# Kernel optimization log

Hardware: AMD Instinct MI355X
Metric: run time of the kernel (lower is better)

The kernel has to match this reference:

```python
import jax, jax.numpy as jnp
import numpy as np

HIDDEN = 2048
INTER = 8192
RETRIEVAL = 128
NUM_EXPERTS = 4096
NUM_KEYS = 64  # sqrt(NUM_EXPERTS)
TOP_K = 8
B, S = 4, 2048


def setup_inputs() -> dict:
    key = jax.random.key(0)
    ks = jax.random.split(key, 8)
    sc = 0.02
    return {
        "hidden_states": jax.random.normal(ks[0], (B, S, HIDDEN), jnp.float32),
        "W_q": jax.random.normal(ks[1], (HIDDEN, RETRIEVAL), jnp.float32) * sc,
        "keys": jax.random.normal(ks[2], (2, RETRIEVAL // 2, NUM_KEYS), jnp.float32) * sc,
        "down_embed": jax.random.normal(ks[3], (NUM_EXPERTS, HIDDEN), jnp.float32) * sc,
        "up_embed": jax.random.normal(ks[4], (NUM_EXPERTS, HIDDEN), jnp.float32) * sc,
        "gate_w": jax.random.normal(ks[5], (HIDDEN, INTER), jnp.float32) * sc,
        "up_w": jax.random.normal(ks[6], (HIDDEN, INTER), jnp.float32) * sc,
        "down_w": jax.random.normal(ks[7], (INTER, HIDDEN), jnp.float32) * sc,
    }


def reference(hidden_states, W_q, keys, down_embed, up_embed, gate_w, up_w, down_w):
    b, s, h = hidden_states.shape
    n = b * s
    # product-key routing (faithful to the source's view(2, N, -1) reshape)
    queries = (hidden_states @ W_q).reshape(2, n, RETRIEVAL // 2)  # [2, N, rd/2]
    routing = jnp.einsum('tnd,tdk->tnk', queries, keys)            # [2, N, num_keys]
    scores2, idx2 = jax.lax.top_k(routing, TOP_K)                  # [2, N, k]
    sx, sy = scores2[0], scores2[1]
    ix, iy = idx2[0], idx2[1]
    all_scores = (sx[:, :, None] + sy[:, None, :]).reshape(n, TOP_K * TOP_K)
    all_idx = (ix[:, :, None] * NUM_KEYS + iy[:, None, :]).reshape(n, TOP_K * TOP_K)
    scores, pk = jax.lax.top_k(all_scores, TOP_K)                  # [N, k]
    indices = jnp.take_along_axis(all_idx, pk, axis=-1)            # [N, k]
    # expert embedding gather + per-token tiny matmuls
    de = down_embed[indices]                                       # [N, k, H]
    ue = up_embed[indices]                                         # [N, k, H]
    x = hidden_states.reshape(n, h)
    ew = jnp.einsum('nh,nkh->nk', x, de)                           # [N, k]
    ew = jax.nn.silu(ew) * jax.nn.softmax(scores, axis=-1)
    experts_states = jnp.einsum('nk,nkh->nh', ew, ue).reshape(b, s, h)
    # dense SwiGLU MLP branch
    mlp = (jax.nn.silu(x @ gate_w) * (x @ up_w)) @ down_w
    return mlp.reshape(b, s, h) + experts_states
```

## Files before the change

kernel.cpp:

```cpp
#include <hip/hip_runtime.h>
#include <cstdint>
#include <cstddef>

#define HIDDEN 2048
#define INTER 8192
#define NTOK 8192
#define RET 128
#define NKEYS 64
#define TOPK 8

typedef __bf16 bf16_t;
typedef bf16_t bf16x8 __attribute__((ext_vector_type(8)));
typedef float floatx4 __attribute__((ext_vector_type(4)));

#define BARRIER() asm volatile("s_barrier" ::: "memory")
#define WAIT_LGKM0()                                     \
  do {                                                   \
    asm volatile("s_waitcnt lgkmcnt(0)" ::: "memory");   \
    __builtin_amdgcn_sched_barrier(0);                   \
  } while (0)
#define WAIT_VM8() asm volatile("s_waitcnt vmcnt(8)" ::: "memory")
#define WAIT_VM4() asm volatile("s_waitcnt vmcnt(4)" ::: "memory")
#define WAIT_VM0() asm volatile("s_waitcnt vmcnt(0)" ::: "memory")

__device__ inline void tile_end_wait(int rem) {
  if (rem >= 3) WAIT_VM8();
  else if (rem == 2) WAIT_VM4();
  else if (rem == 1) WAIT_VM0();
}

__device__ inline unsigned short f2bf(float f) {
  union { float f; unsigned u; } v; v.f = f;
  unsigned r = v.u + 0x7FFFu + ((v.u >> 16) & 1u);
  return (unsigned short)(r >> 16);
}

__device__ inline void gld_lds16(unsigned short* lds, const unsigned short* g) {
  auto* l3 = reinterpret_cast<__attribute__((address_space(3))) unsigned int*>(
      reinterpret_cast<uintptr_t>(lds));
  auto* g1 = reinterpret_cast<const __attribute__((address_space(1))) unsigned int*>(
      reinterpret_cast<uintptr_t>(g));
  __builtin_amdgcn_global_load_lds(g1, l3, 16, 0, 0);
}

__device__ inline void xcd_map(int gx, int gy, int& bx, int& by) {
  if ((gx & 7) != 0) return;
  int lin = by * gx + bx;
  int W = gx >> 3;
  int xcd = lin & 7;
  int j = lin >> 3;
  int r = j / W, c = j % W;
  if (r & 1) c = W - 1 - c;
  bx = xcd * W + c;
  by = r;
}

__device__ inline void stage_op256(unsigned short* ldsbuf, const unsigned short* g,
                                   int rows0, int K, int kt, int tid, int wid) {
#pragma unroll
  for (int i = 0; i < 2; ++i) {
    int c = i * 512 + tid;
    int row = c >> 2;
    int cc = (c & 3) ^ (row & 3) ^ ((row >> 2) & 3);
    gld_lds16(ldsbuf + (size_t)(i * 512 + wid * 64) * 8,
              g + (size_t)(rows0 + row) * K + kt + cc * 8);
  }
}
__device__ inline void stage_op128(unsigned short* ldsbuf, const unsigned short* g,
                                   int rows0, int K, int kt, int tid, int wid) {
  int row = tid >> 2;
  int cc = (tid & 3) ^ (row & 3) ^ ((row >> 2) & 3);
  gld_lds16(ldsbuf + (size_t)(wid * 64) * 8,
            g + (size_t)(rows0 + row) * K + kt + cc * 8);
}

__global__ __launch_bounds__(256) void cvt_bf16(const float* __restrict__ in,
                                                unsigned short* __restrict__ out,
                                                int count4) {
  for (int i = blockIdx.x * blockDim.x + threadIdx.x; i < count4;
       i += gridDim.x * blockDim.x) {
    float4 v = reinterpret_cast<const float4*>(in)[i];
    ushort4 o;
    o.x = f2bf(v.x); o.y = f2bf(v.y); o.z = f2bf(v.z); o.w = f2bf(v.w);
    reinterpret_cast<ushort4*>(out)[i] = o;
  }
}

__global__ __launch_bounds__(256) void transpose_cvt(const float* __restrict__ in,
                                                     unsigned short* __restrict__ out,
                                                     int R, int C) {
  __shared__ float tile[32][33];
  int c0 = blockIdx.x * 32, r0 = blockIdx.y * 32;
  int tx = threadIdx.x, ty = threadIdx.y;
#pragma unroll
  for (int it = 0; it < 4; ++it)
    tile[ty + it * 8][tx] = in[(size_t)(r0 + ty + it * 8) * C + c0 + tx];
  __syncthreads();
#pragma unroll
  for (int it = 0; it < 4; ++it)
    out[(size_t)(c0 + ty + it * 8) * R + r0 + tx] = f2bf(tile[tx][ty + it * 8]);
}

enum { EPI_F32 = 0, EPI_ADDF32 = 3 };

template <int MODE>
__global__ __launch_bounds__(256) void gemm_bt(const unsigned short* __restrict__ A,
                                               const unsigned short* __restrict__ B,
                                               float* __restrict__ Cf,
                                               int M, int N, int K) {
  __shared__ unsigned short As[128 * 64];
  __shared__ unsigned short Bs[128 * 64];
  const int tid = threadIdx.x;
  const int lane = tid & 63, wid = tid >> 6;
  const int wm = wid >> 1, wn = wid & 1;
  int bx = blockIdx.x, by = blockIdx.y;
  xcd_map(gridDim.x, gridDim.y, bx, by);
  const int m0 = by * 128, n0 = bx * 128;
  const int lr = lane & 15, q = lane >> 4;
  const int swz = lr & 7;

  floatx4 acc[4][4];
#pragma unroll
  for (int i = 0; i < 4; ++i)
#pragma unroll
    for (int j = 0; j < 4; ++j) acc[i][j] = (floatx4){0.f, 0.f, 0.f, 0.f};

  for (int k0 = 0; k0 < K; k0 += 64) {
#pragma unroll
    for (int s = 0; s < 4; ++s) {
      int c = s * 256 + wid * 64 + lane;
      int row = c >> 3, cc = (c & 7) ^ (row & 7);
      gld_lds16(&As[(s * 256 + wid * 64) * 8],
                A + (size_t)(m0 + row) * K + k0 + cc * 8);
      gld_lds16(&Bs[(s * 256 + wid * 64) * 8],
                B + (size_t)(n0 + row) * K + k0 + cc * 8);
    }
    __syncthreads();
#pragma unroll
    for (int kc = 0; kc < 2; ++kc) {
      const int coff = ((kc * 4 + q) ^ swz) * 8;
      bf16x8 af[4], bfv[4];
#pragma unroll
      for (int t = 0; t < 4; ++t) {
        af[t] = *reinterpret_cast<const bf16x8*>(
            &As[(wm * 64 + t * 16 + lr) * 64 + coff]);
        bfv[t] = *reinterpret_cast<const bf16x8*>(
            &Bs[(wn * 64 + t * 16 + lr) * 64 + coff]);
      }
#pragma unroll
      for (int i = 0; i < 4; ++i)
#pragma unroll
        for (int j = 0; j < 4; ++j)
          acc[i][j] = __builtin_amdgcn_mfma_f32_16x16x32_bf16(af[i], bfv[j],
                                                              acc[i][j], 0, 0, 0);
    }
    __syncthreads();
  }

#pragma unroll
  for (int i = 0; i < 4; ++i) {
    int rbase = m0 + wm * 64 + i * 16 + q * 4;
#pragma unroll
    for (int j = 0; j < 4; ++j) {
      int col = n0 + wn * 64 + j * 16 + lr;
#pragma unroll
      for (int r = 0; r < 4; ++r) {
        size_t idx = (size_t)(rbase + r) * N + col;
        float v = acc[i][j][r];
        if (MODE == EPI_F32) Cf[idx] = v;
        else Cf[idx] = v + Cf[idx];
      }
    }
  }
}

template <int MODE>
__global__ __launch_bounds__(512, 2) void gemm256(const unsigned short* __restrict__ A,
                                                  const unsigned short* __restrict__ B,
                                                  float* __restrict__ Cf,
                                                  int N, int K) {
  extern __shared__ unsigned short sm[];
  const int tid = threadIdx.x;
  const int lane = tid & 63, wid = tid >> 6;
  const int wm = wid >> 2, wn = wid & 3;
  int bx = blockIdx.x, by = blockIdx.y;
  xcd_map(gridDim.x, gridDim.y, bx, by);
  const int m0 = by * 256, n0 = bx * 256;
  const int lr = lane & 15, q = lane >> 4;
  const int swz = (lr & 3) ^ ((lr >> 2) & 3);
  const int coff = (q ^ swz) * 8;
  unsigned short* Abase = sm;
  unsigned short* Bbase = sm + 32768;
  const int NT = K >> 5;

  floatx4 acc[8][4];
#pragma unroll
  for (int i = 0; i < 8; ++i)
#pragma unroll
    for (int j = 0; j < 4; ++j) acc[i][j] = (floatx4){0.f, 0.f, 0.f, 0.f};

#pragma unroll
  for (int tt = 0; tt < 3; ++tt) {
    stage_op256(Abase + tt * 8192, A, m0, K, tt * 32, tid, wid);
    stage_op256(Bbase + tt * 8192, B, n0, K, tt * 32, tid, wid);
  }
  WAIT_VM8();
  BARRIER();

  for (int t = 0; t < NT; ++t) {
    const int buf = t & 3;
    const unsigned short* As = Abase + buf * 8192;
    const unsigned short* Bs = Bbase + buf * 8192;
    bf16x8 af[4], bfv[4];
#pragma unroll
    for (int m = 0; m < 4; ++m)
      af[m] = *reinterpret_cast<const bf16x8*>(
          &As[(wm * 128 + m * 16 + lr) * 32 + coff]);
#pragma unroll
    for (int n = 0; n < 4; ++n)
      bfv[n] = *reinterpret_cast<const bf16x8*>(
          &Bs[(wn * 64 + n * 16 + lr) * 32 + coff]);
    if (t + 3 < NT)
      stage_op256(Abase + ((t + 3) & 3) * 8192, A, m0, K, (t + 3) * 32, tid, wid);
    BARRIER();
    WAIT_LGKM0();
    __builtin_amdgcn_s_setprio(1);
#pragma unroll
    for (int m = 0; m < 4; ++m)
#pragma unroll
      for (int n = 0; n < 4; ++n)
        acc[m][n] = __builtin_amdgcn_mfma_f32_16x16x32_bf16(af[m], bfv[n],
                                                            acc[m][n], 0, 0, 0);
    __builtin_amdgcn_s_setprio(0);
    __builtin_amdgcn_sched_barrier(0);
    BARRIER();
#pragma unroll
    for (int m = 0; m < 4; ++m)
      af[m] = *reinterpret_cast<const bf16x8*>(
          &As[(wm * 128 + (m + 4) * 16 + lr) * 32 + coff]);
    if (t + 3 < NT)
      stage_op256(Bbase + ((t + 3) & 3) * 8192, B, n0, K, (t + 3) * 32, tid, wid);
    BARRIER();
    WAIT_LGKM0();
    __builtin_amdgcn_s_setprio(1);
#pragma unroll
    for (int m = 0; m < 4; ++m)
#pragma unroll
      for (int n = 0; n < 4; ++n)
        acc[m + 4][n] = __builtin_amdgcn_mfma_f32_16x16x32_bf16(af[m], bfv[n],
                                                                acc[m + 4][n], 0, 0, 0);
    __builtin_amdgcn_s_setprio(0);
    __builtin_amdgcn_sched_barrier(0);
    tile_end_wait(NT - 1 - t);
    BARRIER();
  }

#pragma unroll
  for (int m = 0; m < 8; ++m) {
    int rbase = m0 + wm * 128 + m * 16 + q * 4;
#pragma unroll
    for (int n = 0; n < 4; ++n) {
      int col = n0 + wn * 64 + n * 16 + lr;
#pragma unroll
      for (int r = 0; r < 4; ++r) {
        size_t idx = (size_t)(rbase + r) * N + col;
        float v = acc[m][n][r];
        if (MODE == EPI_F32) Cf[idx] = v;
        else Cf[idx] = v + Cf[idx];
      }
    }
  }
}

__global__ __launch_bounds__(512, 2) void gateup256(const unsigned short* __restrict__ A,
                                                    const unsigned short* __restrict__ Bg,
                                                    const unsigned short* __restrict__ Bu,
                                                    unsigned short* __restrict__ H,
                                                    int N, int K) {
  extern __shared__ unsigned short sm[];
  const int tid = threadIdx.x;
  const int lane = tid & 63, wid = tid >> 6;
  const int wm = wid >> 1, wn = wid & 1;
  int bx = blockIdx.x, by = blockIdx.y;
  xcd_map(gridDim.x, gridDim.y, bx, by);
  const int m0 = by * 256, n0 = bx * 128;
  const int lr = lane & 15, q = lane >> 4;
  const int swz = (lr & 3) ^ ((lr >> 2) & 3);
  const int coff = (q ^ swz) * 8;
  unsigned short* Abase = sm;
  unsigned short* Bgbase = sm + 32768;
  unsigned short* Bubase = sm + 49152;
  const int NT = K >> 5;

  floatx4 accg[4][4], accu[4][4];
#pragma unroll
  for (int i = 0; i < 4; ++i)
#pragma unroll
    for (int j = 0; j < 4; ++j) {
      accg[i][j] = (floatx4){0.f, 0.f, 0.f, 0.f};
      accu[i][j] = (floatx4){0.f, 0.f, 0.f, 0.f};
    }

#pragma unroll
  for (int tt = 0; tt < 3; ++tt) {
    stage_op256(Abase + tt * 8192, A, m0, K, tt * 32, tid, wid);
    stage_op128(Bgbase + tt * 4096, Bg, n0, K, tt * 32, tid, wid);
    stage_op128(Bubase + tt * 4096, Bu, n0, K, tt * 32, tid, wid);
  }
  WAIT_VM8();
  BARRIER();

  for (int t = 0; t < NT; ++t) {
    const int buf = t & 3;
    const unsigned short* As = Abase + buf * 8192;
    const unsigned short* Bgs = Bgbase + buf * 4096;
    const unsigned short* Bus = Bubase + buf * 4096;
    bf16x8 af[2], bg[4], bu[4];
#pragma unroll
    for (int m = 0; m < 2; ++m)
      af[m] = *reinterpret_cast<const bf16x8*>(
          &As[(wm * 64 + m * 16 + lr) * 32 + coff]);
#pragma unroll
    for (int n = 0; n < 4; ++n) {
      bg[n] = *reinterpret_cast<const bf16x8*>(
          &Bgs[(wn * 64 + n * 16 + lr) * 32 + coff]);
      bu[n] = *reinterpret_cast<const bf16x8*>(
          &Bus[(wn * 64 + n * 16 + lr) * 32 + coff]);
    }
    if (t + 3 < NT)
      stage_op256(Abase + ((t + 3) & 3) * 8192, A, m0, K, (t + 3) * 32, tid, wid);
    BARRIER();
    WAIT_LGKM0();
    __builtin_amdgcn_s_setprio(1);
#pragma unroll
    for (int m = 0; m < 2; ++m)
#pragma unroll
      for (int n = 0; n < 4; ++n) {
        accg[m][n] = __builtin_amdgcn_mfma_f32_16x16x32_bf16(af[m], bg[n],
                                                             accg[m][n], 0, 0, 0);
        accu[m][n] = __builtin_amdgcn_mfma_f32_16x16x32_bf16(af[m], bu[n],
                                                             accu[m][n], 0, 0, 0);
      }
    __builtin_amdgcn_s_setprio(0);
    __builtin_amdgcn_sched_barrier(0);
    BARRIER();
#pragma unroll
    for (int m = 0; m < 2; ++m)
      af[m] = *reinterpret_cast<const bf16x8*>(
          &As[(wm * 64 + (m + 2) * 16 + lr) * 32 + coff]);
    if (t + 3 < NT) {
      stage_op128(Bgbase + ((t + 3) & 3) * 4096, Bg, n0, K, (t + 3) * 32, tid, wid);
      stage_op128(Bubase + ((t + 3) & 3) * 4096, Bu, n0, K, (t + 3) * 32, tid, wid);
    }
    BARRIER();
    WAIT_LGKM0();
    __builtin_amdgcn_s_setprio(1);
#pragma unroll
    for (int m = 0; m < 2; ++m)
#pragma unroll
      for (int n = 0; n < 4; ++n) {
        accg[m + 2][n] = __builtin_amdgcn_mfma_f32_16x16x32_bf16(af[m], bg[n],
                                                                 accg[m + 2][n], 0, 0, 0);
        accu[m + 2][n] = __builtin_amdgcn_mfma_f32_16x16x32_bf16(af[m], bu[n],
                                                                 accu[m + 2][n], 0, 0, 0);
      }
    __builtin_amdgcn_s_setprio(0);
    __builtin_amdgcn_sched_barrier(0);
    tile_end_wait(NT - 1 - t);
    BARRIER();
  }

#pragma unroll
  for (int m = 0; m < 4; ++m) {
    int rbase = m0 + wm * 64 + m * 16 + q * 4;
#pragma unroll
    for (int n = 0; n < 4; ++n) {
      int col = n0 + wn * 64 + n * 16 + lr;
#pragma unroll
      for (int r = 0; r < 4; ++r) {
        float g = accg[m][n][r];
        float h = (g / (1.f + __expf(-g))) * accu[m][n][r];
        H[(size_t)(rbase + r) * N + col] = f2bf(h);
      }
    }
  }
}

__global__ __launch_bounds__(256) void routing_kernel(const float* __restrict__ Q,
                                                      const float* __restrict__ keys,
                                                      int* __restrict__ topi,
                                                      float* __restrict__ topw) {
  __shared__ float k0s[64 * 64];
  __shared__ float k1s[64 * 64];
  for (int i = threadIdx.x; i < 64 * 64; i += 256) {
    k0s[i] = keys[i];
    k1s[i] = keys[64 * 64 + i];
  }
  __syncthreads();
  const int lane = threadIdx.x & 63, wid = threadIdx.x >> 6;
  const int gw = blockIdx.x * 4 + wid;
  const float NEG = -__builtin_inff();

  for (int n = gw; n < NTOK; n += 1024) {
    int cbase = (n & 1) * 64;
    float qx = Q[(size_t)(n >> 1) * RET + cbase + lane];
    float qy = Q[(size_t)(NTOK / 2 + (n >> 1)) * RET + cbase + lane];
    float rx = 0.f, ry = 0.f;
#pragma unroll 8
    for (int d = 0; d < 64; ++d) {
      rx += __shfl(qx, d) * k0s[d * 64 + lane];
      ry += __shfl(qy, d) * k1s[d * 64 + lane];
    }
    float mvx = rx, mvy = ry;
    float keptx = 0.f, kepty = 0.f;
    int keptix = 0, keptiy = 0;
#pragma unroll
    for (int a = 0; a < 8; ++a) {
      float v = mvx; int ii = lane;
#pragma unroll
      for (int off = 32; off; off >>= 1) {
        float ov = __shfl_xor(v, off); int oi = __shfl_xor(ii, off);
        if (ov > v || (ov == v && oi < ii)) { v = ov; ii = oi; }
      }
      if (lane == a) { keptx = v; keptix = ii; }
      if (lane == ii) mvx = NEG;
      float w = mvy; int jj = lane;
#pragma unroll
      for (int off = 32; off; off >>= 1) {
        float ow = __shfl_xor(w, off); int oj = __shfl_xor(jj, off);
        if (ow > w || (ow == w && oj < jj)) { w = ow; jj = oj; }
      }
      if (lane == a) { kepty = w; keptiy = jj; }
      if (lane == jj) mvy = NEG;
    }
    float sa = __shfl(keptx, lane >> 3), sb = __shfl(kepty, lane & 7);
    int ia = __shfl(keptix, lane >> 3), ib = __shfl(keptiy, lane & 7);
    float mv = sa + sb;
    int pe = ia * NKEYS + ib;
    float maxs = 0.f, denom = 0.f, kw = 0.f;
    int ke = 0;
#pragma unroll
    for (int a = 0; a < 8; ++a) {
      float v = mv; int pos = lane; int e = pe;
#pragma unroll
      for (int off = 32; off; off >>= 1) {
        float ov = __shfl_xor(v, off);
        int opos = __shfl_xor(pos, off);
        int oe = __shfl_xor(e, off);
        if (ov > v || (ov == v && opos < pos)) { v = ov; pos = opos; e = oe; }
      }
      if (a == 0) maxs = v;
      denom += __expf(v - maxs);
      if (lane == a) { kw = __expf(v - maxs); ke = e; }
      if (lane == pos) mv = NEG;
    }
    if (lane < 8) {
      topw[(size_t)n * 8 + lane] = kw / denom;
      topi[(size_t)n * 8 + lane] = ke;
    }
  }
}

__global__ __launch_bounds__(256) void expert_kernel(const float* __restrict__ X,
                                                     const float* __restrict__ de,
                                                     const float* __restrict__ ue,
                                                     const int* __restrict__ topi,
                                                     const float* __restrict__ topw,
                                                     float* __restrict__ out) {
  const int n = blockIdx.x, t = threadIdx.x;
  const int lane = t & 63, wid = t >> 6;
  __shared__ float red[4][8];
  __shared__ int eidx[8];
  __shared__ float ewt[8];
  if (t < 8) {
    eidx[t] = topi[(size_t)n * 8 + t];
    ewt[t] = topw[(size_t)n * 8 + t];
  }
  __syncthreads();
  const float* x = X + (size_t)n * HIDDEN + t * 8;
  float4 x0 = *(const float4*)x, x1 = *(const float4*)(x + 4);
  float p[8];
#pragma unroll
  for (int k = 0; k < 8; ++k) {
    const float* dr = de + (size_t)eidx[k] * HIDDEN + t * 8;
    float4 d0 = *(const float4*)dr, d1 = *(const float4*)(dr + 4);
    p[k] = x0.x * d0.x + x0.y * d0.y + x0.z * d0.z + x0.w * d0.w +
           x1.x * d1.x + x1.y * d1.y + x1.z * d1.z + x1.w * d1.w;
  }
#pragma unroll
  for (int k = 0; k < 8; ++k)
#pragma unroll
    for (int off = 32; off; off >>= 1) p[k] += __shfl_xor(p[k], off);
  if (lane == 0) {
#pragma unroll
    for (int k = 0; k < 8; ++k) red[wid][k] = p[k];
  }
  __syncthreads();
  float coef[8];
#pragma unroll
  for (int k = 0; k < 8; ++k) {
    float s = red[0][k] + red[1][k] + red[2][k] + red[3][k];
    coef[k] = (s / (1.f + __expf(-s))) * ewt[k];
  }
  float a0 = 0, a1 = 0, a2 = 0, a3 = 0, a4 = 0, a5 = 0, a6 = 0, a7 = 0;
#pragma unroll
  for (int k = 0; k < 8; ++k) {
    const float* ur = ue + (size_t)eidx[k] * HIDDEN + t * 8;
    float4 u0 = *(const float4*)ur, u1 = *(const float4*)(ur + 4);
    float c = coef[k];
    a0 += c * u0.x; a1 += c * u0.y; a2 += c * u0.z; a3 += c * u0.w;
    a4 += c * u1.x; a5 += c * u1.y; a6 += c * u1.z; a7 += c * u1.w;
  }
  float* op = out + (size_t)n * HIDDEN + t * 8;
  *(float4*)op = make_float4(a0, a1, a2, a3);
  *(float4*)(op + 4) = make_float4(a4, a5, a6, a7);
}

extern "C" void kernel_launch(void* const* d_in, const int* in_sizes, int n_in,
                              void* d_out, int out_size, void* d_ws, size_t ws_size,
                              hipStream_t stream) {
  const float* X    = (const float*)d_in[0];
  const float* Wq   = (const float*)d_in[1];
  const float* keys = (const float*)d_in[2];
  const float* de   = (const float*)d_in[3];
  const float* ue   = (const float*)d_in[4];
  const float* Wg   = (const float*)d_in[5];
  const float* Wu   = (const float*)d_in[6];
  const float* Wd   = (const float*)d_in[7];
  float* out = (float*)d_out;

  char* ws = (char*)d_ws;
  size_t o = 0;
  unsigned short* xb  = (unsigned short*)(ws + o); o += (size_t)NTOK * HIDDEN * 2;
  unsigned short* wgt = (unsigned short*)(ws + o); o += (size_t)HIDDEN * INTER * 2;
  unsigned short* wut = (unsigned short*)(ws + o); o += (size_t)HIDDEN * INTER * 2;
  unsigned short* wdt = (unsigned short*)(ws + o); o += (size_t)HIDDEN * INTER * 2;
  unsigned short* hbuf= (unsigned short*)(ws + o); o += (size_t)NTOK * INTER * 2;
  unsigned short* wqt = (unsigned short*)(ws + o); o += (size_t)RET * HIDDEN * 2;
  float* Q            = (float*)(ws + o);          o += (size_t)NTOK * RET * 4;
  int* topi           = (int*)(ws + o);            o += (size_t)NTOK * TOPK * 4;
  float* topw         = (float*)(ws + o);          o += (size_t)NTOK * TOPK * 4;

  static bool attr_done = false;
  if (!attr_done) {
    auto kd = gemm256<EPI_ADDF32>;
    auto kg = gateup256;
    (void)hipFuncSetAttribute(reinterpret_cast<const void*>(kd),
                              hipFuncAttributeMaxDynamicSharedMemorySize, 131072);
    (void)hipFuncSetAttribute(reinterpret_cast<const void*>(kg),
                              hipFuncAttributeMaxDynamicSharedMemorySize, 131072);
    attr_done = true;
  }

  cvt_bf16<<<4096, 256, 0, stream>>>(X, xb, NTOK * HIDDEN / 4);
  transpose_cvt<<<dim3(INTER / 32, HIDDEN / 32), dim3(32, 8), 0, stream>>>(Wg, wgt, HIDDEN, INTER);
  transpose_cvt<<<dim3(INTER / 32, HIDDEN / 32), dim3(32, 8), 0, stream>>>(Wu, wut, HIDDEN, INTER);
  transpose_cvt<<<dim3(HIDDEN / 32, INTER / 32), dim3(32, 8), 0, stream>>>(Wd, wdt, INTER, HIDDEN);
  transpose_cvt<<<dim3(RET / 32, HIDDEN / 32), dim3(32, 8), 0, stream>>>(Wq, wqt, HIDDEN, RET);

  gemm_bt<EPI_F32><<<dim3(1, NTOK / 128), 256, 0, stream>>>(xb, wqt, Q,
                                                            NTOK, RET, HIDDEN);
  routing_kernel<<<256, 256, 0, stream>>>(Q, keys, topi, topw);
  expert_kernel<<<NTOK, 256, 0, stream>>>(X, de, ue, topi, topw, out);

  gateup256<<<dim3(INTER / 128, NTOK / 256), 512, 131072, stream>>>(
      xb, wgt, wut, hbuf, INTER, HIDDEN);
  gemm256<EPI_ADDF32><<<dim3(HIDDEN / 256, NTOK / 256), 512, 131072, stream>>>(
      hbuf, wdt, out, HIDDEN, INTER);
}
```

Before: 1.563 ms.

## Restructure GEMMs to BK=64 triple-buffered pipeline with smaller N tiles

Both the gate/up GEMM and the down-projection GEMM now use a 64-wide K step with three LDS slots instead of a 32-wide K step with four buffers, and an 8-way XOR swizzle. The down GEMM shrinks its tile from 256x256 to 256x128 and the gate/up GEMM from N=128 to N=64, doubling the grid. The aim is fewer barriers per K element and more blocks for better CU coverage. In exchange, data reuse per block is lower and each block needs more dynamic LDS (147456 bytes), which may limit occupancy to one block per CU.

Measured after the change: 1.501 ms. -4.0%, faster.

```diff
diff --git a/kernel.cpp b/kernel.cpp
--- a/kernel.cpp
+++ b/kernel.cpp
@@ -19,13 +19,11 @@
     asm volatile("s_waitcnt lgkmcnt(0)" ::: "memory");   \
     __builtin_amdgcn_sched_barrier(0);                   \
   } while (0)
-#define WAIT_VM8() asm volatile("s_waitcnt vmcnt(8)" ::: "memory")
-#define WAIT_VM4() asm volatile("s_waitcnt vmcnt(4)" ::: "memory")
+#define WAIT_VM6() asm volatile("s_waitcnt vmcnt(6)" ::: "memory")
 #define WAIT_VM0() asm volatile("s_waitcnt vmcnt(0)" ::: "memory")
 
-__device__ inline void tile_end_wait(int rem) {
-  if (rem >= 3) WAIT_VM8();
-  else if (rem == 2) WAIT_VM4();
+__device__ inline void tile_end_wait3(int rem) {
+  if (rem >= 2) WAIT_VM6();
   else if (rem == 1) WAIT_VM0();
 }
 
@@ -55,23 +53,16 @@
   by = r;
 }
 
-__device__ inline void stage_op256(unsigned short* ldsbuf, const unsigned short* g,
-                                   int rows0, int K, int kt, int tid, int wid) {
-#pragma unroll
-  for (int i = 0; i < 2; ++i) {
-    int c = i * 512 + tid;
-    int row = c >> 2;
-    int cc = (c & 3) ^ (row & 3) ^ ((row >> 2) & 3);
-    gld_lds16(ldsbuf + (size_t)(i * 512 + wid * 64) * 8,
+template <int ROWS>
+__device__ inline void stage_tile(unsigned short* ldsbuf, const unsigned short* g,
+                                  int rows0, int K, int kt, int tid, int wid) {
+#pragma unroll
+  for (int s = 0; s < ROWS / 64; ++s) {
+    int c = s * 512 + tid;
+    int row = c >> 3, cc = (c & 7) ^ (row & 7);
+    gld_lds16(ldsbuf + (size_t)(s * 512 + wid * 64) * 8,
               g + (size_t)(rows0 + row) * K + kt + cc * 8);
   }
-}
-__device__ inline void stage_op128(unsigned short* ldsbuf, const unsigned short* g,
-                                   int rows0, int K, int kt, int tid, int wid) {
-  int row = tid >> 2;
-  int cc = (tid & 3) ^ (row & 3) ^ ((row >> 2) & 3);
-  gld_lds16(ldsbuf + (size_t)(wid * 64) * 8,
-            g + (size_t)(rows0 + row) * K + kt + cc * 8);
 }
 
 __global__ __launch_bounds__(256) void cvt_bf16(const float* __restrict__ in,
@@ -175,89 +166,77 @@
 }
 
 template <int MODE>
-__global__ __launch_bounds__(512, 2) void gemm256(const unsigned short* __restrict__ A,
+__global__ __launch_bounds__(512, 2) void gemm_dp(const unsigned short* __restrict__ A,
                                                   const unsigned short* __restrict__ B,
                                                   float* __restrict__ Cf,
                                                   int N, int K) {
   extern __shared__ unsigned short sm[];
   const int tid = threadIdx.x;
   const int lane = tid & 63, wid = tid >> 6;
-  const int wm = wid >> 2, wn = wid & 3;
+  const int wm = wid >> 1, wn = wid & 1;
   int bx = blockIdx.x, by = blockIdx.y;
   xcd_map(gridDim.x, gridDim.y, bx, by);
-  const int m0 = by * 256, n0 = bx * 256;
+  const int m0 = by * 256, n0 = bx * 128;
   const int lr = lane & 15, q = lane >> 4;
-  const int swz = (lr & 3) ^ ((lr >> 2) & 3);
-  const int coff = (q ^ swz) * 8;
-  unsigned short* Abase = sm;
-  unsigned short* Bbase = sm + 32768;
-  const int NT = K >> 5;
-
-  floatx4 acc[8][4];
-#pragma unroll
-  for (int i = 0; i < 8; ++i)
+  const int swz = lr & 7;
+  const int SLOT = 24576;
+  const int NT = K >> 6;
+
+  floatx4 acc[4][4];
+#pragma unroll
+  for (int i = 0; i < 4; ++i)
 #pragma unroll
     for (int j = 0; j < 4; ++j) acc[i][j] = (floatx4){0.f, 0.f, 0.f, 0.f};
 
 #pragma unroll
-  for (int tt = 0; tt < 3; ++tt) {
-    stage_op256(Abase + tt * 8192, A, m0, K, tt * 32, tid, wid);
-    stage_op256(Bbase + tt * 8192, B, n0, K, tt * 32, tid, wid);
-  }
-  WAIT_VM8();
+  for (int tt = 0; tt < 2; ++tt) {
+    unsigned short* slot = sm + tt * SLOT;
+    stage_tile<256>(slot, A, m0, K, tt * 64, tid, wid);
+    stage_tile<128>(slot + 16384, B, n0, K, tt * 64, tid, wid);
+  }
+  WAIT_VM6();
   BARRIER();
 
   for (int t = 0; t < NT; ++t) {
-    const int buf = t & 3;
-    const unsigned short* As = Abase + buf * 8192;
-    const unsigned short* Bs = Bbase + buf * 8192;
-    bf16x8 af[4], bfv[4];
-#pragma unroll
-    for (int m = 0; m < 4; ++m)
-      af[m] = *reinterpret_cast<const bf16x8*>(
-          &As[(wm * 128 + m * 16 + lr) * 32 + coff]);
-#pragma unroll
-    for (int n = 0; n < 4; ++n)
-      bfv[n] = *reinterpret_cast<const bf16x8*>(
-          &Bs[(wn * 64 + n * 16 + lr) * 32 + coff]);
-    if (t + 3 < NT)
-      stage_op256(Abase + ((t + 3) & 3) * 8192, A, m0, K, (t + 3) * 32, tid, wid);
-    BARRIER();
-    WAIT_LGKM0();
-    __builtin_amdgcn_s_setprio(1);
-#pragma unroll
-    for (int m = 0; m < 4; ++m)
+    unsigned short* slot = sm + (t % 3) * SLOT;
+    const unsigned short* As = slot;
+    const unsigned short* Bs = slot + 16384;
+    unsigned short* nslot = sm + ((t + 2) % 3) * SLOT;
+#pragma unroll
+    for (int kc = 0; kc < 2; ++kc) {
+      const int coff = ((kc * 4 + q) ^ swz) * 8;
+      bf16x8 af[4], bfv[4];
+#pragma unroll
+      for (int m = 0; m < 4; ++m)
+        af[m] = *reinterpret_cast<const bf16x8*>(
+            &As[(wm * 64 + m * 16 + lr) * 64 + coff]);
 #pragma unroll
       for (int n = 0; n < 4; ++n)
-        acc[m][n] = __builtin_amdgcn_mfma_f32_16x16x32_bf16(af[m], bfv[n],
-                                                            acc[m][n], 0, 0, 0);
-    __builtin_amdgcn_s_setprio(0);
-    __builtin_amdgcn_sched_barrier(0);
-    BARRIER();
-#pragma unroll
-    for (int m = 0; m < 4; ++m)
-      af[m] = *reinterpret_cast<const bf16x8*>(
-          &As[(wm * 128 + (m + 4) * 16 + lr) * 32 + coff]);
-    if (t + 3 < NT)
-      stage_op256(Bbase + ((t + 3) & 3) * 8192, B, n0, K, (t + 3) * 32, tid, wid);
-    BARRIER();
-    WAIT_LGKM0();
-    __builtin_amdgcn_s_setprio(1);
-#pragma unroll
-    for (int m = 0; m < 4; ++m)
-#pragma unroll
-      for (int n = 0; n < 4; ++n)
-        acc[m + 4][n] = __builtin_amdgcn_mfma_f32_16x16x32_bf16(af[m], bfv[n],
-                                                                acc[m + 4][n], 0, 0, 0);
-    __builtin_amdgcn_s_setprio(0);
-    __builtin_amdgcn_sched_barrier(0);
-    tile_end_wait(NT - 1 - t);
-    BARRIER();
-  }
-
-#pragma unroll
-  for (int m = 0; m < 8; ++m) {
-    int rbase = m0 + wm * 128 + m * 16 + q * 4;
+        bfv[n] = *reinterpret_cast<const bf16x8*>(
+            &Bs[(wn * 64 + n * 16 + lr) * 64 + coff]);
+      if (t + 2 < NT) {
+        if (kc == 0) stage_tile<256>(nslot, A, m0, K, (t + 2) * 64, tid, wid);
+        else stage_tile<128>(nslot + 16384, B, n0, K, (t + 2) * 64, tid, wid);
+      }
+      BARRIER();
+      WAIT_LGKM0();
+      __builtin_amdgcn_s_setprio(1);
+#pragma unroll
+      for (int m = 0; m < 4; ++m)
+#pragma unroll
+        for (int n = 0; n < 4; ++n)
+          acc[m][n] = __builtin_amdgcn_mfma_f32_16x16x32_bf16(af[m], bfv[n],
+                                                              acc[m][n], 0, 0, 0);
+      __builtin_amdgcn_s_setprio(0);
+      __builtin_amdgcn_sched_barrier(0);
+      if (kc == 1) tile_end_wait3(NT - 1 - t);
+      BARRIER();
+    }
+  }
+
+#pragma unroll
+  for (int m = 0; m < 4; ++m) {
+    int rbase = m0 + wm * 64 + m * 16 + q * 4;
 #pragma unroll
     for (int n = 0; n < 4; ++n) {
       int col = n0 + wn * 64 + n * 16 + lr;
@@ -272,7 +251,7 @@
   }
 }
 
-__global__ __launch_bounds__(512, 2) void gateup256(const unsigned short* __restrict__ A,
+__global__ __launch_bounds__(512, 2) void gateup_p3(const unsigned short* __restrict__ A,
                                                     const unsigned short* __restrict__ Bg,
                                                     const unsigned short* __restrict__ Bu,
                                                     unsigned short* __restrict__ H,
@@ -283,99 +262,85 @@
   const int wm = wid >> 1, wn = wid & 1;
   int bx = blockIdx.x, by = blockIdx.y;
   xcd_map(gridDim.x, gridDim.y, bx, by);
-  const int m0 = by * 256, n0 = bx * 128;
+  const int m0 = by * 256, n0 = bx * 64;
   const int lr = lane & 15, q = lane >> 4;
-  const int swz = (lr & 3) ^ ((lr >> 2) & 3);
-  const int coff = (q ^ swz) * 8;
-  unsigned short* Abase = sm;
-  unsigned short* Bgbase = sm + 32768;
-  unsigned short* Bubase = sm + 49152;
-  const int NT = K >> 5;
-
-  floatx4 accg[4][4], accu[4][4];
+  const int swz = lr & 7;
+  const int SLOT = 24576;
+  const int NT = K >> 6;
+
+  floatx4 accg[4][2], accu[4][2];
 #pragma unroll
   for (int i = 0; i < 4; ++i)
 #pragma unroll
-    for (int j = 0; j < 4; ++j) {
+    for (int j = 0; j < 2; ++j) {
       accg[i][j] = (floatx4){0.f, 0.f, 0.f, 0.f};
       accu[i][j] = (floatx4){0.f, 0.f, 0.f, 0.f};
     }
 
 #pragma unroll
-  for (int tt = 0; tt < 3; ++tt) {
-    stage_op256(Abase + tt * 8192, A, m0, K, tt * 32, tid, wid);
-    stage_op128(Bgbase + tt * 4096, Bg, n0, K, tt * 32, tid, wid);
-    stage_op128(Bubase + tt * 4096, Bu, n0, K, tt * 32, tid, wid);
-  }
-  WAIT_VM8();
+  for (int tt = 0; tt < 2; ++tt) {
+    unsigned short* slot = sm + tt * SLOT;
+    stage_tile<256>(slot, A, m0, K, tt * 64, tid, wid);
+    stage_tile<64>(slot + 16384, Bg, n0, K, tt * 64, tid, wid);
+    stage_tile<64>(slot + 20480, Bu, n0, K, tt * 64, tid, wid);
+  }
+  WAIT_VM6();
   BARRIER();
 
   for (int t = 0; t < NT; ++t) {
-    const int buf = t & 3;
-    const unsigned short* As = Abase + buf * 8192;
-    const unsigned short* Bgs = Bgbase + buf * 4096;
-    const unsigned short* Bus = Bubase + buf * 4096;
-    bf16x8 af[2], bg[4], bu[4];
-#pragma unroll
-    for (int m = 0; m < 2; ++m)
-      af[m] = *reinterpret_cast<const bf16x8*>(
-          &As[(wm * 64 + m * 16 + lr) * 32 + coff]);
-#pragma unroll
-    for (int n = 0; n < 4; ++n) {
-      bg[n] = *reinterpret_cast<const bf16x8*>(
-          &Bgs[(wn * 64 + n * 16 + lr) * 32 + coff]);
-      bu[n] = *reinterpret_cast<const bf16x8*>(
-          &Bus[(wn * 64 + n * 16 + lr) * 32 + coff]);
-    }
-    if (t + 3 < NT)
-      stage_op256(Abase + ((t + 3) & 3) * 8192, A, m0, K, (t + 3) * 32, tid, wid);
-    BARRIER();
-    WAIT_LGKM0();
-    __builtin_amdgcn_s_setprio(1);
-#pragma unroll
-    for (int m = 0; m < 2; ++m)
-#pragma unroll
-      for (int n = 0; n < 4; ++n) {
-        accg[m][n] = __builtin_amdgcn_mfma_f32_16x16x32_bf16(af[m], bg[n],
-                                                             accg[m][n], 0, 0, 0);
-        accu[m][n] = __builtin_amdgcn_mfma_f32_16x16x32_bf16(af[m], bu[n],
-                                                             accu[m][n], 0, 0, 0);
-      }
-    __builtin_amdgcn_s_setprio(0);
-    __builtin_amdgcn_sched_barrier(0);
-    BARRIER();
-#pragma unroll
-    for (int m = 0; m < 2; ++m)
-      af[m] = *reinterpret_cast<const bf16x8*>(
-          &As[(wm * 64 + (m + 2) * 16 + lr) * 32 + coff]);
-    if (t + 3 < NT) {
-      stage_op128(Bgbase + ((t + 3) & 3) * 4096, Bg, n0, K, (t + 3) * 32, tid, wid);
-      stage_op128(Bubase + ((t + 3) & 3) * 4096, Bu, n0, K, (t + 3) * 32, tid, wid);
-    }
-    BARRIER();
-    WAIT_LGKM0();
-    __builtin_amdgcn_s_setprio(1);
-#pragma unroll
-    for (int m = 0; m < 2; ++m)
-#pragma unroll
-      for (int n = 0; n < 4; ++n) {
-        accg[m + 2][n] = __builtin_amdgcn_mfma_f32_16x16x32_bf16(af[m], bg[n],
-                                                                 accg[m + 2][n], 0, 0, 0);
-        accu[m + 2][n] = __builtin_amdgcn_mfma_f32_16x16x32_bf16(af[m], bu[n],
-                                                                 accu[m + 2][n], 0, 0, 0);
-      }
-    __builtin_amdgcn_s_setprio(0);
-    __builtin_amdgcn_sched_barrier(0);
-    tile_end_wait(NT - 1 - t);
-    BARRIER();
+    unsigned short* slot = sm + (t % 3) * SLOT;
+    const unsigned short* As = slot;
+    const unsigned short* Bgs = slot + 16384;
+    const unsigned short* Bus = slot + 20480;
+    unsigned short* nslot = sm + ((t + 2) % 3) * SLOT;
+#pragma unroll
+    for (int kc = 0; kc < 2; ++kc) {
+      const int coff = ((kc * 4 + q) ^ swz) * 8;
+      bf16x8 af[4], bg[2], bu[2];
+#pragma unroll
+      for (int m = 0; m < 4; ++m)
+        af[m] = *reinterpret_cast<const bf16x8*>(
+            &As[(wm * 64 + m * 16 + lr) * 64 + coff]);
+#pragma unroll
+      for (int n = 0; n < 2; ++n) {
+        bg[n] = *reinterpret_cast<const bf16x8*>(
+            &Bgs[(wn * 32 + n * 16 + lr) * 64 + coff]);
+        bu[n] = *reinterpret_cast<const bf16x8*>(
+            &Bus[(wn * 32 + n * 16 + lr) * 64 + coff]);
+      }
+      if (t + 2 < NT) {
+        if (kc == 0) {
+          stage_tile<256>(nslot, A, m0, K, (t + 2) * 64, tid, wid);
+        } else {
+          stage_tile<64>(nslot + 16384, Bg, n0, K, (t + 2) * 64, tid, wid);
+          stage_tile<64>(nslot + 20480, Bu, n0, K, (t + 2) * 64, tid, wid);
+        }
+      }
+      BARRIER();
+      WAIT_LGKM0();
+      __builtin_amdgcn_s_setprio(1);
+#pragma unroll
+      for (int m = 0; m < 4; ++m)
+#pragma unroll
+        for (int n = 0; n < 2; ++n) {
+          accg[m][n] = __builtin_amdgcn_mfma_f32_16x16x32_bf16(af[m], bg[n],
+                                                               accg[m][n], 0, 0, 0);
+          accu[m][n] = __builtin_amdgcn_mfma_f32_16x16x32_bf16(af[m], bu[n],
+                                                               accu[m][n], 0, 0, 0);
+        }
+      __builtin_amdgcn_s_setprio(0);
+      __builtin_amdgcn_sched_barrier(0);
+      if (kc == 1) tile_end_wait3(NT - 1 - t);
+      BARRIER();
+    }
   }
 
 #pragma unroll
   for (int m = 0; m < 4; ++m) {
     int rbase = m0 + wm * 64 + m * 16 + q * 4;
 #pragma unroll
-    for (int n = 0; n < 4; ++n) {
-      int col = n0 + wn * 64 + n * 16 + lr;
+    for (int n = 0; n < 2; ++n) {
+      int col = n0 + wn * 32 + n * 16 + lr;
 #pragma unroll
       for (int r = 0; r < 4; ++r) {
         float g = accg[m][n][r];
@@ -543,12 +508,12 @@
 
   static bool attr_done = false;
   if (!attr_done) {
-    auto kd = gemm256<EPI_ADDF32>;
-    auto kg = gateup256;
+    auto kd = gemm_dp<EPI_ADDF32>;
+    auto kg = gateup_p3;
     (void)hipFuncSetAttribute(reinterpret_cast<const void*>(kd),
-                              hipFuncAttributeMaxDynamicSharedMemorySize, 131072);
+                              hipFuncAttributeMaxDynamicSharedMemorySize, 147456);
     (void)hipFuncSetAttribute(reinterpret_cast<const void*>(kg),
-                              hipFuncAttributeMaxDynamicSharedMemorySize, 131072);
+                              hipFuncAttributeMaxDynamicSharedMemorySize, 147456);
     attr_done = true;
   }
 
@@ -563,8 +528,8 @@
   routing_kernel<<<256, 256, 0, stream>>>(Q, keys, topi, topw);
   expert_kernel<<<NTOK, 256, 0, stream>>>(X, de, ue, topi, topw, out);
 
-  gateup256<<<dim3(INTER / 128, NTOK / 256), 512, 131072, stream>>>(
+  gateup_p3<<<dim3(INTER / 64, NTOK / 256), 512, 147456, stream>>>(
       xb, wgt, wut, hbuf, INTER, HIDDEN);
-  gemm256<EPI_ADDF32><<<dim3(HIDDEN / 256, NTOK / 256), 512, 131072, stream>>>(
+  gemm_dp<EPI_ADDF32><<<dim3(HIDDEN / 128, NTOK / 256), 512, 147456, stream>>>(
       hbuf, wdt, out, HIDDEN, INTER);
 }
```
